# Optimization experiments

Measured on AMD Instinct MI355X. Metric: run time of the kernel, lower is better.

The kernel has to match this reference:

```python
import jax, jax.numpy as jnp
import numpy as np

NEG_SLOPE = 0.2  # HANConv default negative_slope
N_NODES = 100000
N_REL = 8
N_EDGES = 200000
N_LABEL = 131072
C_IN = 128
H1 = 128
H2 = 128


def _segment_softmax(logits, seg, num_segments):
    # PyG softmax(src, index): exp(src - max_per_seg) / (sum_per_seg + 1e-16)
    m = jax.ops.segment_max(logits, seg, num_segments=num_segments)
    m = jnp.where(jnp.isfinite(m), m, 0.0)  # empty segments -> 0
    e = jnp.exp(logits - m[seg])
    s = jax.ops.segment_sum(e, seg, num_segments=num_segments)
    return e / (s[seg] + 1e-16)


def _han_layer(x, edge_index, proj_w, proj_b, att_src, att_dst, q, klin_w, klin_b):
    # x: [N, Cin]; edge_index: [R, 2, E]; att_src/att_dst: [R, D]; klin_w: [D, D] (torch [out,in])
    N = x.shape[0]
    h = x @ proj_w + proj_b            # [N, D] shared projection for node type 'node'
    a_src = h @ att_src.T              # [N, R] per-node src attention logits
    a_dst = h @ att_dst.T              # [N, R]

    def per_rel(eidx, a_s, a_d):
        src, dst = eidx[0], eidx[1]
        alpha = jax.nn.leaky_relu(a_s[src] + a_d[dst], NEG_SLOPE)     # [E]
        alpha = _segment_softmax(alpha, dst, N)                        # softmax over in-neighbors
        out = jax.ops.segment_sum(alpha[:, None] * h[src], dst, num_segments=N)  # [N, D]
        return jax.nn.relu(out)        # HANConv applies relu per edge-type output

    outs = jax.vmap(per_rel, in_axes=(0, 1, 1))(edge_index, a_src, a_dst)  # [R, N, D]
    # semantic attention across edge types (group())
    score = jnp.einsum('d,rd->r', q, jnp.tanh(outs @ klin_w.T + klin_b).mean(axis=1))
    attn = jax.nn.softmax(score)       # [R]
    return jnp.einsum('r,rnd->nd', attn, outs)


def setup_inputs() -> dict:
    key = jax.random.key(0)
    ks = jax.random.split(key, 24)
    f32 = jnp.float32

    def lin_w(k, fin, fout):
        return (jax.random.normal(k, (fin, fout), f32) / np.sqrt(fin)).astype(f32)

    inp = {
        'x': jax.random.normal(ks[0], (N_NODES, C_IN), f32),
        'edge_index': jax.random.randint(ks[1], (N_REL, 2, N_EDGES), 0, N_NODES, jnp.int32),
        'edge_label_index': jax.random.randint(ks[2], (2, N_LABEL), 0, N_NODES, jnp.int32),
        # HANConv layer 1 params
        'w1': lin_w(ks[3], C_IN, H1), 'b1': jnp.zeros((H1,), f32),
        'asrc1': jax.random.normal(ks[4], (N_REL, H1), f32) / np.sqrt(H1),
        'adst1': jax.random.normal(ks[5], (N_REL, H1), f32) / np.sqrt(H1),
        'q1': jax.random.normal(ks[6], (H1,), f32) / np.sqrt(H1),
        'kw1': lin_w(ks[7], H1, H1).T, 'kb1': jnp.zeros((H1,), f32),
        # HANConv layer 2 params
        'w2': lin_w(ks[8], H1, H2), 'b2': jnp.zeros((H2,), f32),
        'asrc2': jax.random.normal(ks[9], (N_REL, H2), f32) / np.sqrt(H2),
        'adst2': jax.random.normal(ks[10], (N_REL, H2), f32) / np.sqrt(H2),
        'q2': jax.random.normal(ks[11], (H2,), f32) / np.sqrt(H2),
        'kw2': lin_w(ks[12], H2, H2).T, 'kb2': jnp.zeros((H2,), f32),
        # link-score head
        'post_w': lin_w(ks[13], H2, 2), 'post_b': jnp.zeros((2,), f32),
    }
    return inp


def reference(x, edge_index, edge_label_index,
              w1, b1, asrc1, adst1, q1, kw1, kb1,
              w2, b2, asrc2, adst2, q2, kw2, kb2,
              post_w, post_b):
    h = jax.nn.relu(_han_layer(x, edge_index, w1, b1, asrc1, adst1, q1, kw1, kb1))
    h = jax.nn.relu(_han_layer(h, edge_index, w2, b2, asrc2, adst2, q2, kw2, kb2))
    h_had = h[edge_label_index[0]] * h[edge_label_index[1]]   # [L, H2]
    logits = h_had @ post_w + post_b                          # [L, 2]
    return logits.sum(axis=-1)                                # [L]
```

## Files before the change

### kernel.cpp

```cpp
#include <hip/hip_runtime.h>

#define NN 100000
#define NR 8
#define NE 200000
#define NL 131072
#define NSEG (NR*NN)
#define NB_SCAN 782
#define NPAD (NB_SCAN*1024)

typedef __attribute__((ext_vector_type(8))) short short8;
typedef __attribute__((ext_vector_type(4))) float floatx4;

__device__ __forceinline__ unsigned short f2bf(float f) {
    unsigned u = __float_as_uint(f);
    unsigned r = (u + 0x7fff + ((u >> 16) & 1)) >> 16;
    return (unsigned short)r;
}
__device__ __forceinline__ float bf2f(unsigned short s) {
    return __uint_as_float(((unsigned)s) << 16);
}

__global__ void transpose128(const float* __restrict__ in, float* __restrict__ out) {
    int idx = blockIdx.x * 256 + threadIdx.x;
    int j = idx >> 7, k = idx & 127;
    out[idx] = in[k * 128 + j];
}

__global__ void cast_bf16(const float* __restrict__ src, unsigned short* __restrict__ dst) {
    size_t idx = ((size_t)blockIdx.x * 256 + threadIdx.x) * 4;
    float4 v = *(const float4*)(src + idx);
    ushort4 o;
    o.x = f2bf(v.x); o.y = f2bf(v.y); o.z = f2bf(v.z); o.w = f2bf(v.w);
    *(ushort4*)(dst + idx) = o;
}

__global__ void hist_kernel(const int* __restrict__ ei, int* __restrict__ counts) {
    int idx = blockIdx.x * 256 + threadIdx.x;
    if (idx >= NR * NE) return;
    int r = idx / NE, e = idx - r * NE;
    int dst = ei[(size_t)r * 2 * NE + NE + e];
    atomicAdd(&counts[r * NN + dst], 1);
}

__global__ __launch_bounds__(256) void scan_k1(const int* __restrict__ counts,
                                               int* __restrict__ rowptr,
                                               int* __restrict__ bsums) {
    __shared__ int wsum[4];
    int t = threadIdx.x, lane = t & 63, w = t >> 6;
    int base = blockIdx.x * 1024 + t * 4;
    int c0 = counts[base], c1 = counts[base + 1], c2 = counts[base + 2], c3 = counts[base + 3];
    int s = c0 + c1 + c2 + c3;
    int inc = s;
#pragma unroll
    for (int off = 1; off < 64; off <<= 1) { int v = __shfl_up(inc, off); if (lane >= off) inc += v; }
    if (lane == 63) wsum[w] = inc;
    __syncthreads();
    int wbase = 0;
    for (int k = 0; k < w; ++k) wbase += wsum[k];
    int ex = wbase + inc - s;
    rowptr[base]     = ex;
    rowptr[base + 1] = ex + c0;
    rowptr[base + 2] = ex + c0 + c1;
    rowptr[base + 3] = ex + c0 + c1 + c2;
    if (t == 255) bsums[blockIdx.x] = wbase + inc;
}

__global__ __launch_bounds__(256) void scan_k2(int* __restrict__ bsums, int nb) {
    __shared__ int wsum[4];
    __shared__ int carry_s;
    int t = threadIdx.x, lane = t & 63, w = t >> 6;
    if (t == 0) carry_s = 0;
    __syncthreads();
    for (int base = 0; base < nb; base += 256) {
        int i = base + t;
        int v = (i < nb) ? bsums[i] : 0;
        int inc = v;
#pragma unroll
        for (int off = 1; off < 64; off <<= 1) { int u = __shfl_up(inc, off); if (lane >= off) inc += u; }
        if (lane == 63) wsum[w] = inc;
        __syncthreads();
        int wbase = carry_s;
        for (int k = 0; k < w; ++k) wbase += wsum[k];
        if (i < nb) bsums[i] = wbase + inc - v;
        __syncthreads();
        if (t == 0) carry_s += wsum[0] + wsum[1] + wsum[2] + wsum[3];
        __syncthreads();
    }
}

__global__ void scan_k3(int* __restrict__ rowptr, const int* __restrict__ bsums) {
    int i = blockIdx.x * 256 + threadIdx.x;
    if (i <= NSEG) rowptr[i] += bsums[i >> 10];
}

__global__ void fill_kernel(const int* __restrict__ ei, const int* __restrict__ rowptr,
                            int* __restrict__ cursor, int* __restrict__ es_raw) {
    int idx = blockIdx.x * 256 + threadIdx.x;
    if (idx >= NR * NE) return;
    int r = idx / NE, e = idx - r * NE;
    int src = ei[(size_t)r * 2 * NE + e];
    int dst = ei[(size_t)r * 2 * NE + NE + e];
    int g = r * NN + dst;
    int pos = rowptr[g] + atomicAdd(&cursor[g], 1);
    es_raw[2 * pos] = src;
}

__global__ __launch_bounds__(256, 3) void gemm_proj(
    const float* __restrict__ A, const float* __restrict__ B,
    const float* __restrict__ bias, float* __restrict__ out, int nrows)
{
    __shared__ float As[128][36];
    __shared__ float Bs[128][36];
    const int tid = threadIdx.x;
    const int row0 = blockIdx.x * 128;
    const int cg = tid & 15;
    const int nb = (tid >> 4) * 8;

    float acc[8][8];
#pragma unroll
    for (int i = 0; i < 8; ++i)
#pragma unroll
        for (int j = 0; j < 8; ++j) acc[i][j] = 0.f;

    for (int k0 = 0; k0 < 128; k0 += 32) {
#pragma unroll
        for (int i = 0; i < 4; ++i) {
            int fi = tid + i * 256;
            int rw = fi >> 3, kq = fi & 7;
            int n = row0 + rw;
            float4 v = make_float4(0.f, 0.f, 0.f, 0.f);
            if (n < nrows) v = *(const float4*)(A + (size_t)n * 128 + k0 + kq * 4);
            *(float4*)&As[rw][kq * 4] = v;
            float4 w = *(const float4*)(B + rw * 128 + k0 + kq * 4);
            *(float4*)&Bs[rw][kq * 4] = w;
        }
        __syncthreads();
#pragma unroll 2
        for (int kq = 0; kq < 8; ++kq) {
            float4 wv[8];
#pragma unroll
            for (int j = 0; j < 8; ++j) wv[j] = *(const float4*)&Bs[cg + 16 * j][kq * 4];
#pragma unroll
            for (int i = 0; i < 8; ++i) {
                float4 xv = *(const float4*)&As[nb + i][kq * 4];
#pragma unroll
                for (int j = 0; j < 8; ++j)
                    acc[i][j] += xv.x * wv[j].x + xv.y * wv[j].y
                               + xv.z * wv[j].z + xv.w * wv[j].w;
            }
        }
        __syncthreads();
    }
#pragma unroll
    for (int i = 0; i < 8; ++i) {
        int n = row0 + nb + i;
        if (n < nrows) {
#pragma unroll
            for (int j = 0; j < 8; ++j) {
                int d = cg + 16 * j;
                out[(size_t)n * 128 + d] = acc[i][j] + bias[d];
            }
        }
    }
}

__global__ __launch_bounds__(256) void fused_score2(
    const int* __restrict__ rowptr, const int2* __restrict__ es,
    const unsigned short* __restrict__ h16,
    const unsigned short* __restrict__ kw16, const float* __restrict__ kb,
    const float* __restrict__ q, float* __restrict__ score)
{
    __shared__ unsigned short Os[64][136];
    __shared__ float redbuf[4];
    const int t = threadIdx.x;
    const int r = blockIdx.y;
    const int row0 = blockIdx.x * 64;
    const int l = t & 7, ng = t >> 3;

#pragma unroll
    for (int pass = 0; pass < 2; ++pass) {
        int nl = pass * 32 + ng;
        int n = row0 + nl;
        float acc[16];
#pragma unroll
        for (int i = 0; i < 16; ++i) acc[i] = 0.f;
        if (n < NN) {
            int g = r * NN + n;
            int p0 = rowptr[g], p1 = rowptr[g + 1];
            for (int e = p0; e < p1; ++e) {
                int2 ep = es[e];
                float al = __int_as_float(ep.y);
                const unsigned short* hp = h16 + (size_t)ep.x * 128 + l * 16;
                short8 h0 = *(const short8*)hp;
                short8 h1 = *(const short8*)(hp + 8);
#pragma unroll
                for (int i = 0; i < 8; ++i) acc[i]     += al * bf2f((unsigned short)h0[i]);
#pragma unroll
                for (int i = 0; i < 8; ++i) acc[8 + i] += al * bf2f((unsigned short)h1[i]);
            }
        }
        unsigned short ov[16];
#pragma unroll
        for (int i = 0; i < 16; ++i) ov[i] = f2bf(fmaxf(acc[i], 0.f));
        *(short8*)&Os[nl][l * 16]     = *(short8*)&ov[0];
        *(short8*)&Os[nl][l * 16 + 8] = *(short8*)&ov[8];
    }
    __syncthreads();

    const int wave = t >> 6, lane = t & 63;
    const int quad = lane >> 4, l16 = lane & 15;
    short8 a[4];
#pragma unroll
    for (int kc = 0; kc < 4; ++kc)
        a[kc] = *(const short8*)&Os[wave * 16 + l16][quad * 8 + kc * 32];

    float s = 0.f;
#pragma unroll
    for (int dt = 0; dt < 8; ++dt) {
        const unsigned short* brow = kw16 + (size_t)(dt * 16 + l16) * 128 + quad * 8;
        floatx4 accv = {0.f, 0.f, 0.f, 0.f};
#pragma unroll
        for (int kc = 0; kc < 4; ++kc) {
            short8 b = *(const short8*)(brow + kc * 32);
            accv = __builtin_amdgcn_mfma_f32_16x16x32_bf16(a[kc], b, accv, 0, 0, 0);
        }
        int d = dt * 16 + l16;
        float kbv = kb[d], qv = q[d];
#pragma unroll
        for (int reg = 0; reg < 4; ++reg) {
            int node = row0 + wave * 16 + quad * 4 + reg;
            if (node < NN) {
                float y = accv[reg] + kbv;
                float e2 = __expf(2.f * y);
                float tn = 1.f - 2.f * __builtin_amdgcn_rcpf(e2 + 1.f);
                s += tn * qv;
            }
        }
    }
    for (int off = 32; off > 0; off >>= 1) s += __shfl_down(s, off);
    if (lane == 0) redbuf[wave] = s;
    __syncthreads();
    if (t == 0) atomicAdd(score + r, redbuf[0] + redbuf[1] + redbuf[2] + redbuf[3]);
}

__global__ __launch_bounds__(256) void att_kernel(
    const float* __restrict__ h, const float* __restrict__ asrc_w,
    const float* __restrict__ adst_w, float* __restrict__ a_src,
    float* __restrict__ a_dst, unsigned short* __restrict__ h16)
{
    __shared__ float hs[16][128];
    int n0 = blockIdx.x * 16;
#pragma unroll
    for (int i = 0; i < 2; ++i) {
        int fi = threadIdx.x + i * 256;
        int n = fi >> 5, kq = fi & 31;
        float4 v = make_float4(0.f, 0.f, 0.f, 0.f);
        if (n0 + n < NN) v = *(const float4*)(h + (size_t)(n0 + n) * 128 + kq * 4);
        *(float4*)&hs[n][kq * 4] = v;
    }
    __syncthreads();
    int n = threadIdx.x >> 4, rr = threadIdx.x & 15;
    int r = rr & 7; int isd = rr >> 3;
    const float* w = (isd ? adst_w : asrc_w) + r * 128;
    float acc = 0.f;
#pragma unroll
    for (int kq = 0; kq < 32; ++kq) {
        float4 hv = *(const float4*)&hs[n][kq * 4];
        float4 wv = ((const float4*)w)[kq];
        acc += hv.x * wv.x + hv.y * wv.y + hv.z * wv.z + hv.w * wv.w;
    }
    if (n0 + n < NN) (isd ? a_dst : a_src)[r * NN + n0 + n] = acc;

    int dq = rr * 8;
    if (n0 + n < NN) {
        unsigned short ov[8];
#pragma unroll
        for (int k = 0; k < 8; ++k) ov[k] = f2bf(hs[n][dq + k]);
        *(short8*)(h16 + (size_t)(n0 + n) * 128 + dq) = *(short8*)ov;
    }
}

__global__ void softmax_csr(const int* __restrict__ rowptr, int2* __restrict__ es,
                            const float* __restrict__ a_src, const float* __restrict__ a_dst)
{
    int g = blockIdx.x * 256 + threadIdx.x;
    if (g >= NSEG) return;
    int p0 = rowptr[g], p1 = rowptr[g + 1];
    if (p0 == p1) return;
    int r = g / NN;
    float ad = a_dst[g];
    const float* as = a_src + (size_t)r * NN;
    float m = -1e30f;
    for (int i = p0; i < p1; ++i) {
        float l = as[es[i].x] + ad;
        l = l > 0.f ? l : 0.2f * l;
        es[i].y = __float_as_int(l);
        m = fmaxf(m, l);
    }
    float s = 0.f;
    for (int i = p0; i < p1; ++i) {
        float e = __expf(__int_as_float(es[i].y) - m);
        es[i].y = __float_as_int(e);
        s += e;
    }
    float inv = __builtin_amdgcn_rcpf(s + 1e-16f);
    for (int i = p0; i < p1; ++i)
        es[i].y = __float_as_int(__int_as_float(es[i].y) * inv);
}

__global__ __launch_bounds__(256) void combine_csr(
    const int* __restrict__ rowptr, const int2* __restrict__ es,
    const float* __restrict__ h, const float* __restrict__ score,
    float* __restrict__ comb)
{
    __shared__ float attn[NR];
    __shared__ float lds[4][64][17];
    int t = threadIdx.x;
    if (t == 0) {
        float sc[NR]; float m = -1e30f;
        for (int r = 0; r < NR; ++r) { sc[r] = score[r] * (1.0f / NN); m = fmaxf(m, sc[r]); }
        float den = 0.f;
        for (int r = 0; r < NR; ++r) { sc[r] = __expf(sc[r] - m); den += sc[r]; }
        for (int r = 0; r < NR; ++r) attn[r] = sc[r] / den;
    }
    __syncthreads();

    int nl = t >> 6;
    int n = blockIdx.x * 4 + nl;
    int L = t & 63;
    int r = L >> 3;
    int d0 = (L & 7) * 16;
    float a[16];
#pragma unroll
    for (int i = 0; i < 16; ++i) a[i] = 0.f;
    {
        int g = r * NN + n;
        int p0 = rowptr[g], p1 = rowptr[g + 1];
        for (int e = p0; e < p1; ++e) {
            int2 ep = es[e];
            float al = __int_as_float(ep.y);
            const float* hp = h + (size_t)ep.x * 128 + d0;
            float4 v0 = *(const float4*)hp;
            float4 v1 = *(const float4*)(hp + 4);
            float4 v2 = *(const float4*)(hp + 8);
            float4 v3 = *(const float4*)(hp + 12);
            a[0]+=al*v0.x; a[1]+=al*v0.y; a[2]+=al*v0.z;  a[3]+=al*v0.w;
            a[4]+=al*v1.x; a[5]+=al*v1.y; a[6]+=al*v1.z;  a[7]+=al*v1.w;
            a[8]+=al*v2.x; a[9]+=al*v2.y; a[10]+=al*v2.z; a[11]+=al*v2.w;
            a[12]+=al*v3.x;a[13]+=al*v3.y;a[14]+=al*v3.z; a[15]+=al*v3.w;
        }
    }
    float w = attn[r];
    float* dst = &lds[nl][L][0];
#pragma unroll
    for (int i = 0; i < 16; ++i) dst[i] = w * fmaxf(a[i], 0.f);
    __syncthreads();

    int o = L >> 3, j = L & 7;
    float s0 = 0.f, s1 = 0.f;
#pragma unroll
    for (int rr = 0; rr < NR; ++rr) {
        s0 += lds[nl][rr * 8 + o][2 * j];
        s1 += lds[nl][rr * 8 + o][2 * j + 1];
    }
    *(float2*)(comb + (size_t)n * 128 + 2 * L) = make_float2(s0, s1);
}

__global__ __launch_bounds__(256) void head_kernel(
    const float* __restrict__ hfin, const int* __restrict__ eli,
    const float* __restrict__ pw, const float* __restrict__ pb,
    float* __restrict__ out)
{
    int t = threadIdx.x;
    int l = blockIdx.x * 4 + (t >> 6);
    int d0 = (t & 63) * 2;
    int a = eli[l], b = eli[NL + l];
    float2 ha = *(const float2*)(hfin + (size_t)a * 128 + d0);
    float2 hb = *(const float2*)(hfin + (size_t)b * 128 + d0);
    float w0 = pw[d0 * 2] + pw[d0 * 2 + 1];
    float w1 = pw[d0 * 2 + 2] + pw[d0 * 2 + 3];
    float v = ha.x * hb.x * w0 + ha.y * hb.y * w1;
    for (int off = 32; off > 0; off >>= 1) v += __shfl_down(v, off);
    if ((t & 63) == 0) out[l] = v + pb[0] + pb[1];
}

extern "C" void kernel_launch(void* const* d_in, const int* in_sizes, int n_in,
                              void* d_out, int out_size, void* d_ws, size_t ws_size,
                              hipStream_t stream)
{
    const float* x     = (const float*)d_in[0];
    const int*   ei    = (const int*)d_in[1];
    const int*   eli   = (const int*)d_in[2];
    const float* w1    = (const float*)d_in[3];
    const float* b1    = (const float*)d_in[4];
    const float* asrc1 = (const float*)d_in[5];
    const float* adst1 = (const float*)d_in[6];
    const float* q1    = (const float*)d_in[7];
    const float* kw1   = (const float*)d_in[8];
    const float* kb1   = (const float*)d_in[9];
    const float* w2    = (const float*)d_in[10];
    const float* b2    = (const float*)d_in[11];
    const float* asrc2 = (const float*)d_in[12];
    const float* adst2 = (const float*)d_in[13];
    const float* q2    = (const float*)d_in[14];
    const float* kw2   = (const float*)d_in[15];
    const float* kb2   = (const float*)d_in[16];
    const float* pw    = (const float*)d_in[17];
    const float* pb    = (const float*)d_in[18];
    float* out = (float*)d_out;

    float* ws      = (float*)d_ws;
    float* hA      = ws;
    float* hB      = ws + 12800000ull;
    float* a_src   = ws + 25600000ull;
    float* a_dst   = ws + 26400000ull;
    int2*  es      = (int2*)(ws + 27200000ull);
    int*   rowptr  = (int*)(ws + 30400000ull);
    int*   counts  = (int*)(ws + 31200768ull);
    int*   bsums   = (int*)(ws + 32001536ull);
    float* score   = ws + 32002560ull;
    float* wt      = ws + 32002624ull;
    unsigned short* kw16 = (unsigned short*)(ws + 32019008ull);
    unsigned short* h16 = (unsigned short*)hB;

    hipMemsetAsync(counts, 0, NPAD * sizeof(int), stream);
    hist_kernel<<<6250, 256, 0, stream>>>(ei, counts);
    scan_k1<<<NB_SCAN, 256, 0, stream>>>(counts, rowptr, bsums);
    scan_k2<<<1, 256, 0, stream>>>(bsums, NB_SCAN);
    scan_k3<<<3126, 256, 0, stream>>>(rowptr, bsums);
    hipMemsetAsync(counts, 0, NPAD * sizeof(int), stream);
    fill_kernel<<<6250, 256, 0, stream>>>(ei, rowptr, counts, (int*)es);

    for (int layer = 0; layer < 2; ++layer) {
        const float* Ain  = layer ? hB : x;
        const float* W    = layer ? w2 : w1;
        const float* bb   = layer ? b2 : b1;
        const float* as_w = layer ? asrc2 : asrc1;
        const float* ad_w = layer ? adst2 : adst1;
        const float* qq   = layer ? q2 : q1;
        const float* kw   = layer ? kw2 : kw1;
        const float* kb   = layer ? kb2 : kb1;

        transpose128<<<64, 256, 0, stream>>>(W, wt);
        gemm_proj<<<782, 256, 0, stream>>>(Ain, wt, bb, hA, NN);
        cast_bf16<<<16, 256, 0, stream>>>(kw, kw16);
        att_kernel<<<6250, 256, 0, stream>>>(hA, as_w, ad_w, a_src, a_dst, h16);
        softmax_csr<<<3125, 256, 0, stream>>>(rowptr, es, a_src, a_dst);
        hipMemsetAsync(score, 0, 64 * sizeof(float), stream);
        fused_score2<<<dim3(1563, NR), 256, 0, stream>>>(rowptr, es, h16,
                                                         kw16, kb, qq, score);
        combine_csr<<<25000, 256, 0, stream>>>(rowptr, es, hA, score, hB);
    }
    head_kernel<<<32768, 256, 0, stream>>>(hB, eli, pw, pb, out);
}
```

Measured before the change: 1.438 ms.

## Switch CSR aggregation to edge-parallel LDS atomics per 64-node tile

Packs the low 6 bits of the destination node into the upper bits of each CSR source entry. The score and combine kernels then walk a tile's contiguous edge range edge-parallel and accumulate into LDS with float atomics, where before each thread walked one node's neighbours. This removes the load imbalance from variable in-degree and the idle lanes on nodes with few neighbours. combine2 now processes 64 nodes and all relations per block with far fewer blocks. The cost is LDS atomic contention and a nondeterministic summation order.

```diff
diff --git a/kernel.cpp b/kernel.cpp
--- a/kernel.cpp
+++ b/kernel.cpp
@@ -7,6 +7,7 @@
 #define NSEG (NR*NN)
 #define NB_SCAN 782
 #define NPAD (NB_SCAN*1024)
+#define SRCMASK 0xFFFFF
 
 typedef __attribute__((ext_vector_type(8))) short short8;
 typedef __attribute__((ext_vector_type(4))) float floatx4;
@@ -102,7 +103,7 @@
     int dst = ei[(size_t)r * 2 * NE + NE + e];
     int g = r * NN + dst;
     int pos = rowptr[g] + atomicAdd(&cursor[g], 1);
-    es_raw[2 * pos] = src;
+    es_raw[2 * pos] = src | ((dst & 63) << 20);
 }
 
 __global__ __launch_bounds__(256, 3) void gemm_proj(
@@ -164,46 +165,57 @@
     }
 }
 
-__global__ __launch_bounds__(256) void fused_score2(
+__global__ __launch_bounds__(256) void fused_score3(
     const int* __restrict__ rowptr, const int2* __restrict__ es,
     const unsigned short* __restrict__ h16,
     const unsigned short* __restrict__ kw16, const float* __restrict__ kb,
     const float* __restrict__ q, float* __restrict__ score)
 {
-    __shared__ unsigned short Os[64][136];
+    __shared__ float Os[64][129];
+    __shared__ int rp[65];
     __shared__ float redbuf[4];
     const int t = threadIdx.x;
     const int r = blockIdx.y;
     const int row0 = blockIdx.x * 64;
-    const int l = t & 7, ng = t >> 3;
-
-#pragma unroll
-    for (int pass = 0; pass < 2; ++pass) {
-        int nl = pass * 32 + ng;
-        int n = row0 + nl;
-        float acc[16];
-#pragma unroll
-        for (int i = 0; i < 16; ++i) acc[i] = 0.f;
-        if (n < NN) {
-            int g = r * NN + n;
-            int p0 = rowptr[g], p1 = rowptr[g + 1];
-            for (int e = p0; e < p1; ++e) {
-                int2 ep = es[e];
-                float al = __int_as_float(ep.y);
-                const unsigned short* hp = h16 + (size_t)ep.x * 128 + l * 16;
-                short8 h0 = *(const short8*)hp;
-                short8 h1 = *(const short8*)(hp + 8);
-#pragma unroll
-                for (int i = 0; i < 8; ++i) acc[i]     += al * bf2f((unsigned short)h0[i]);
-#pragma unroll
-                for (int i = 0; i < 8; ++i) acc[8 + i] += al * bf2f((unsigned short)h1[i]);
-            }
-        }
-        unsigned short ov[16];
-#pragma unroll
-        for (int i = 0; i < 16; ++i) ov[i] = f2bf(fmaxf(acc[i], 0.f));
-        *(short8*)&Os[nl][l * 16]     = *(short8*)&ov[0];
-        *(short8*)&Os[nl][l * 16 + 8] = *(short8*)&ov[8];
+
+    if (t < 65) rp[t] = rowptr[r * NN + min(row0 + t, NN)];
+    for (int i = t; i < 64 * 129; i += 256) ((float*)Os)[i] = 0.f;
+    __syncthreads();
+
+    const int ebase = rp[0], eend = rp[64];
+    const int l = t & 7;
+    int e = ebase + (t >> 3);
+    for (; e + 32 < eend; e += 64) {
+        int2 e0 = es[e], e1 = es[e + 32];
+        int w0 = e0.x >> 20, s0 = e0.x & SRCMASK;
+        int w1 = e1.x >> 20, s1 = e1.x & SRCMASK;
+        float a0 = __int_as_float(e0.y), a1 = __int_as_float(e1.y);
+        const unsigned short* hp0 = h16 + (size_t)s0 * 128 + l * 16;
+        const unsigned short* hp1 = h16 + (size_t)s1 * 128 + l * 16;
+        short8 x0 = *(const short8*)hp0, x1 = *(const short8*)(hp0 + 8);
+        short8 y0 = *(const short8*)hp1, y1 = *(const short8*)(hp1 + 8);
+        float* o0 = &Os[w0][l * 16];
+        float* o1 = &Os[w1][l * 16];
+#pragma unroll
+        for (int i = 0; i < 8; ++i) atomicAdd(&o0[i],     a0 * bf2f((unsigned short)x0[i]));
+#pragma unroll
+        for (int i = 0; i < 8; ++i) atomicAdd(&o0[8 + i], a0 * bf2f((unsigned short)x1[i]));
+#pragma unroll
+        for (int i = 0; i < 8; ++i) atomicAdd(&o1[i],     a1 * bf2f((unsigned short)y0[i]));
+#pragma unroll
+        for (int i = 0; i < 8; ++i) atomicAdd(&o1[8 + i], a1 * bf2f((unsigned short)y1[i]));
+    }
+    if (e < eend) {
+        int2 e0 = es[e];
+        int w0 = e0.x >> 20, s0 = e0.x & SRCMASK;
+        float a0 = __int_as_float(e0.y);
+        const unsigned short* hp0 = h16 + (size_t)s0 * 128 + l * 16;
+        short8 x0 = *(const short8*)hp0, x1 = *(const short8*)(hp0 + 8);
+        float* o0 = &Os[w0][l * 16];
+#pragma unroll
+        for (int i = 0; i < 8; ++i) atomicAdd(&o0[i],     a0 * bf2f((unsigned short)x0[i]));
+#pragma unroll
+        for (int i = 0; i < 8; ++i) atomicAdd(&o0[8 + i], a0 * bf2f((unsigned short)x1[i]));
     }
     __syncthreads();
 
@@ -211,8 +223,13 @@
     const int quad = lane >> 4, l16 = lane & 15;
     short8 a[4];
 #pragma unroll
-    for (int kc = 0; kc < 4; ++kc)
-        a[kc] = *(const short8*)&Os[wave * 16 + l16][quad * 8 + kc * 32];
+    for (int kc = 0; kc < 4; ++kc) {
+        short8 av;
+#pragma unroll
+        for (int j = 0; j < 8; ++j)
+            av[j] = (short)f2bf(fmaxf(Os[wave * 16 + l16][quad * 8 + kc * 32 + j], 0.f));
+        a[kc] = av;
+    }
 
     float s = 0.f;
 #pragma unroll
@@ -292,7 +309,7 @@
     const float* as = a_src + (size_t)r * NN;
     float m = -1e30f;
     for (int i = p0; i < p1; ++i) {
-        float l = as[es[i].x] + ad;
+        float l = as[es[i].x & SRCMASK] + ad;
         l = l > 0.f ? l : 0.2f * l;
         es[i].y = __float_as_int(l);
         m = fmaxf(m, l);
@@ -308,62 +325,110 @@
         es[i].y = __float_as_int(__int_as_float(es[i].y) * inv);
 }
 
-__global__ __launch_bounds__(256) void combine_csr(
+__global__ __launch_bounds__(256) void combine2(
     const int* __restrict__ rowptr, const int2* __restrict__ es,
     const float* __restrict__ h, const float* __restrict__ score,
     float* __restrict__ comb)
 {
+    __shared__ float Os[64][129];
+    __shared__ int rp[65];
     __shared__ float attn[NR];
-    __shared__ float lds[4][64][17];
-    int t = threadIdx.x;
+    const int t = threadIdx.x;
+    const int row0 = blockIdx.x * 64;
+
     if (t == 0) {
         float sc[NR]; float m = -1e30f;
-        for (int r = 0; r < NR; ++r) { sc[r] = score[r] * (1.0f / NN); m = fmaxf(m, sc[r]); }
+        for (int rr = 0; rr < NR; ++rr) { sc[rr] = score[rr] * (1.0f / NN); m = fmaxf(m, sc[rr]); }
         float den = 0.f;
-        for (int r = 0; r < NR; ++r) { sc[r] = __expf(sc[r] - m); den += sc[r]; }
-        for (int r = 0; r < NR; ++r) attn[r] = sc[r] / den;
-    }
-    __syncthreads();
-
-    int nl = t >> 6;
-    int n = blockIdx.x * 4 + nl;
-    int L = t & 63;
-    int r = L >> 3;
-    int d0 = (L & 7) * 16;
-    float a[16];
-#pragma unroll
-    for (int i = 0; i < 16; ++i) a[i] = 0.f;
-    {
-        int g = r * NN + n;
-        int p0 = rowptr[g], p1 = rowptr[g + 1];
-        for (int e = p0; e < p1; ++e) {
-            int2 ep = es[e];
-            float al = __int_as_float(ep.y);
-            const float* hp = h + (size_t)ep.x * 128 + d0;
-            float4 v0 = *(const float4*)hp;
-            float4 v1 = *(const float4*)(hp + 4);
-            float4 v2 = *(const float4*)(hp + 8);
-            float4 v3 = *(const float4*)(hp + 12);
-            a[0]+=al*v0.x; a[1]+=al*v0.y; a[2]+=al*v0.z;  a[3]+=al*v0.w;
-            a[4]+=al*v1.x; a[5]+=al*v1.y; a[6]+=al*v1.z;  a[7]+=al*v1.w;
-            a[8]+=al*v2.x; a[9]+=al*v2.y; a[10]+=al*v2.z; a[11]+=al*v2.w;
-            a[12]+=al*v3.x;a[13]+=al*v3.y;a[14]+=al*v3.z; a[15]+=al*v3.w;
-        }
-    }
-    float w = attn[r];
-    float* dst = &lds[nl][L][0];
-#pragma unroll
-    for (int i = 0; i < 16; ++i) dst[i] = w * fmaxf(a[i], 0.f);
-    __syncthreads();
-
-    int o = L >> 3, j = L & 7;
-    float s0 = 0.f, s1 = 0.f;
-#pragma unroll
-    for (int rr = 0; rr < NR; ++rr) {
-        s0 += lds[nl][rr * 8 + o][2 * j];
-        s1 += lds[nl][rr * 8 + o][2 * j + 1];
-    }
-    *(float2*)(comb + (size_t)n * 128 + 2 * L) = make_float2(s0, s1);
+        for (int rr = 0; rr < NR; ++rr) { sc[rr] = __expf(sc[rr] - m); den += sc[rr]; }
+        for (int rr = 0; rr < NR; ++rr) attn[rr] = sc[rr] / den;
+    }
+    for (int i = t; i < 64 * 129; i += 256) ((float*)Os)[i] = 0.f;
+
+    const int l = t & 7;
+    const int frow = t & 63, fd0 = (t >> 6) * 32;
+    float acc[32];
+#pragma unroll
+    for (int i = 0; i < 32; ++i) acc[i] = 0.f;
+
+    for (int r = 0; r < NR; ++r) {
+        if (t < 65) rp[t] = rowptr[r * NN + min(row0 + t, NN)];
+        __syncthreads();
+        int ebase = rp[0], eend = rp[64];
+        int e = ebase + (t >> 3);
+        for (; e + 32 < eend; e += 64) {
+            int2 e0 = es[e], e1 = es[e + 32];
+            int w0 = e0.x >> 20, s0 = e0.x & SRCMASK;
+            int w1 = e1.x >> 20, s1 = e1.x & SRCMASK;
+            float a0 = __int_as_float(e0.y), a1 = __int_as_float(e1.y);
+            const float* hp0 = h + (size_t)s0 * 128 + l * 16;
+            const float* hp1 = h + (size_t)s1 * 128 + l * 16;
+            float4 u0 = *(const float4*)hp0,       u1 = *(const float4*)(hp0 + 4);
+            float4 u2 = *(const float4*)(hp0 + 8), u3 = *(const float4*)(hp0 + 12);
+            float4 v0 = *(const float4*)hp1,       v1 = *(const float4*)(hp1 + 4);
+            float4 v2 = *(const float4*)(hp1 + 8), v3 = *(const float4*)(hp1 + 12);
+            float* o0 = &Os[w0][l * 16];
+            float* o1 = &Os[w1][l * 16];
+            atomicAdd(&o0[0],  a0 * u0.x); atomicAdd(&o0[1],  a0 * u0.y);
+            atomicAdd(&o0[2],  a0 * u0.z); atomicAdd(&o0[3],  a0 * u0.w);
+            atomicAdd(&o0[4],  a0 * u1.x); atomicAdd(&o0[5],  a0 * u1.y);
+            atomicAdd(&o0[6],  a0 * u1.z); atomicAdd(&o0[7],  a0 * u1.w);
+            atomicAdd(&o0[8],  a0 * u2.x); atomicAdd(&o0[9],  a0 * u2.y);
+            atomicAdd(&o0[10], a0 * u2.z); atomicAdd(&o0[11], a0 * u2.w);
+            atomicAdd(&o0[12], a0 * u3.x); atomicAdd(&o0[13], a0 * u3.y);
+            atomicAdd(&o0[14], a0 * u3.z); atomicAdd(&o0[15], a0 * u3.w);
+            atomicAdd(&o1[0],  a1 * v0.x); atomicAdd(&o1[1],  a1 * v0.y);
+            atomicAdd(&o1[2],  a1 * v0.z); atomicAdd(&o1[3],  a1 * v0.w);
+            atomicAdd(&o1[4],  a1 * v1.x); atomicAdd(&o1[5],  a1 * v1.y);
+            atomicAdd(&o1[6],  a1 * v1.z); atomicAdd(&o1[7],  a1 * v1.w);
+            atomicAdd(&o1[8],  a1 * v2.x); atomicAdd(&o1[9],  a1 * v2.y);
+            atomicAdd(&o1[10], a1 * v2.z); atomicAdd(&o1[11], a1 * v2.w);
+            atomicAdd(&o1[12], a1 * v3.x); atomicAdd(&o1[13], a1 * v3.y);
+            atomicAdd(&o1[14], a1 * v3.z); atomicAdd(&o1[15], a1 * v3.w);
+        }
+        if (e < eend) {
+            int2 e0 = es[e];
+            int w0 = e0.x >> 20, s0 = e0.x & SRCMASK;
+            float a0 = __int_as_float(e0.y);
+            const float* hp0 = h + (size_t)s0 * 128 + l * 16;
+            float4 u0 = *(const float4*)hp0,       u1 = *(const float4*)(hp0 + 4);
+            float4 u2 = *(const float4*)(hp0 + 8), u3 = *(const float4*)(hp0 + 12);
+            float* o0 = &Os[w0][l * 16];
+            atomicAdd(&o0[0],  a0 * u0.x); atomicAdd(&o0[1],  a0 * u0.y);
+            atomicAdd(&o0[2],  a0 * u0.z); atomicAdd(&o0[3],  a0 * u0.w);
+            atomicAdd(&o0[4],  a0 * u1.x); atomicAdd(&o0[5],  a0 * u1.y);
+            atomicAdd(&o0[6],  a0 * u1.z); atomicAdd(&o0[7],  a0 * u1.w);
+            atomicAdd(&o0[8],  a0 * u2.x); atomicAdd(&o0[9],  a0 * u2.y);
+            atomicAdd(&o0[10], a0 * u2.z); atomicAdd(&o0[11], a0 * u2.w);
+            atomicAdd(&o0[12], a0 * u3.x); atomicAdd(&o0[13], a0 * u3.y);
+            atomicAdd(&o0[14], a0 * u3.z); atomicAdd(&o0[15], a0 * u3.w);
+        }
+        __syncthreads();
+        float w = attn[r];
+        if (r < NR - 1) {
+#pragma unroll
+            for (int i = 0; i < 32; ++i) {
+                acc[i] += w * fmaxf(Os[frow][fd0 + i], 0.f);
+                Os[frow][fd0 + i] = 0.f;
+            }
+        } else {
+#pragma unroll
+            for (int i = 0; i < 32; ++i) acc[i] += w * fmaxf(Os[frow][fd0 + i], 0.f);
+        }
+    }
+    __syncthreads();
+#pragma unroll
+    for (int i = 0; i < 32; ++i) Os[frow][fd0 + i] = acc[i];
+    __syncthreads();
+    int node = row0 + (t >> 2), d0 = (t & 3) * 32;
+    if (node < NN) {
+#pragma unroll
+        for (int k = 0; k < 8; ++k) {
+            float4 v = make_float4(Os[t >> 2][d0 + 4 * k],     Os[t >> 2][d0 + 4 * k + 1],
+                                   Os[t >> 2][d0 + 4 * k + 2], Os[t >> 2][d0 + 4 * k + 3]);
+            *(float4*)(comb + (size_t)node * 128 + d0 + 4 * k) = v;
+        }
+    }
 }
 
 __global__ __launch_bounds__(256) void head_kernel(
@@ -447,9 +512,9 @@
         att_kernel<<<6250, 256, 0, stream>>>(hA, as_w, ad_w, a_src, a_dst, h16);
         softmax_csr<<<3125, 256, 0, stream>>>(rowptr, es, a_src, a_dst);
         hipMemsetAsync(score, 0, 64 * sizeof(float), stream);
-        fused_score2<<<dim3(1563, NR), 256, 0, stream>>>(rowptr, es, h16,
+        fused_score3<<<dim3(1563, NR), 256, 0, stream>>>(rowptr, es, h16,
                                                          kw16, kb, qq, score);
-        combine_csr<<<25000, 256, 0, stream>>>(rowptr, es, hA, score, hB);
+        combine2<<<1563, 256, 0, stream>>>(rowptr, es, hA, score, hB);
     }
     head_kernel<<<32768, 256, 0, stream>>>(hB, eli, pw, pb, out);
 }
```

Result: slower. 5.262 ms (+266.0%).
